# Kernel tuning notes

Hardware: AMD Instinct MI355X
Metric: run time of the kernel (lower is better)

Reference implementation:

```python
import jax, jax.numpy as jnp
import numpy as np

# Grid constants from point_cloud_range and PILLAR_SIZE (KITTI PointPillars defaults)
PX, PY, PZ = 0.16, 0.16, 4.0
X0, Y0, Z0 = 0.0, -39.68, -3.0
NX, NY, NZ = 432, 496, 1
X_OFF = PX / 2 + X0
Y_OFF = PY / 2 + Y0
Z_OFF = PZ / 2 + Z0
B = 8          # batch size
P = 96000      # total pillars across batch
M = 32         # max points per pillar
CIN = 10       # 4 base + 3 cluster + 3 center
COUT = 64      # FILTERS[-1]
BN_EPS = 1e-3


def setup_inputs() -> dict:
    key = jax.random.key(0)
    k1, k2, k3, k4, k5, k6 = jax.random.split(key, 6)
    pillars = jax.random.normal(k1, (P, M, 4), dtype=jnp.float32)
    b = jax.random.randint(k2, (P,), 0, B, dtype=jnp.int32)
    z = jnp.zeros((P,), dtype=jnp.int32)  # nz == 1
    y = jax.random.randint(k3, (P,), 0, NY, dtype=jnp.int32)
    x = jax.random.randint(k4, (P,), 0, NX, dtype=jnp.int32)
    coords = jnp.stack([b, z, y, x], axis=1)  # (P, 4) as [batch, z, y, x]
    num_points = jax.random.randint(k5, (P,), 1, M + 1, dtype=jnp.int32)
    W = jax.random.normal(k6, (CIN, COUT), dtype=jnp.float32) * 0.05
    gamma = jnp.ones((COUT,), dtype=jnp.float32)
    beta = jnp.zeros((COUT,), dtype=jnp.float32)
    return {"pillars": pillars, "coords": coords, "num_points": num_points,
            "W": W, "gamma": gamma, "beta": beta}


def _pfe_forward(pillars, W, gamma, beta, coords, num_points):
    # --- feature augmentation ---
    abs_xyz = pillars[:, :, :3]                                   # (P, M, 3)
    n = num_points.astype(pillars.dtype)[:, None, None]
    mean_xyz = jnp.sum(abs_xyz, axis=1, keepdims=True) / n        # (P, 1, 3)
    xyz_to_cluster = abs_xyz - mean_xyz                           # (P, M, 3)
    cz = coords[:, 1].astype(pillars.dtype)
    cy = coords[:, 2].astype(pillars.dtype)
    cx = coords[:, 3].astype(pillars.dtype)
    centers = jnp.stack([cx * PX + X_OFF, cy * PY + Y_OFF, cz * PZ + Z_OFF], axis=-1)
    xyz_to_center = abs_xyz - centers[:, None, :]                 # (P, M, 3)
    feats = jnp.concatenate([pillars, xyz_to_cluster, xyz_to_center], axis=-1)  # (P, M, 10)

    # --- PFNLayer: linear (no bias) + BatchNorm1d (train-mode batch stats) + ReLU + max over points ---
    h = jnp.einsum("pmi,io->pmo", feats, W)                       # (P, M, COUT)
    mu = jnp.mean(h, axis=(0, 1))
    var = jnp.var(h, axis=(0, 1))                                 # biased, like torch BN
    h = (h - mu) * jax.lax.rsqrt(var + BN_EPS) * gamma + beta
    h = jax.nn.relu(h)
    pv = jnp.max(h, axis=1)                                       # (P, COUT)

    # --- scatter pillar features to dense BEV grid ---
    cell = coords[:, 1] + coords[:, 2] * NX + coords[:, 3]        # z + y*nx + x
    flat = coords[:, 0] * (NZ * NY * NX) + cell                   # (P,)
    bev = jnp.zeros((B * NZ * NY * NX, COUT), dtype=pv.dtype).at[flat].set(pv)
    bev = bev.reshape(B, NZ * NY * NX, COUT).transpose(0, 2, 1)   # (B, C, nz*ny*nx)
    return bev.reshape(B, COUT * NZ, NY, NX)


def reference(pillars, coords, num_points, W, gamma, beta):
    return _pfe_forward(pillars, W, gamma, beta, coords, num_points)
```

## Files before the change

### kernel.cpp

```cpp
#include <hip/hip_runtime.h>

#define NPILLARS 96000
#define MPTS 32
#define NCHAN 64
#define NXC 432
#define NYC 496
#define NB 8
#define NCELLS (NXC*NYC)
#define NBLK 1024
#define PXc 0.16f
#define PYc 0.16f
#define PZc 4.0f
#define XOFF (0.08f)
#define YOFF (0.08f - 39.68f)
#define ZOFF (2.0f - 3.0f)
#define BN_EPS 1e-3f

typedef __attribute__((ext_vector_type(8))) short short8;
typedef __attribute__((ext_vector_type(16))) float float16;
typedef __attribute__((ext_vector_type(4))) float natf4;

__device__ __forceinline__ short f2bf(float x) {
    union { float f; unsigned u; } v; v.f = x;
    unsigned r = v.u + 0x7FFFu + ((v.u >> 16) & 1u);
    return (short)(r >> 16);
}

#define PAIRS(Q) \
 Q(0,0,0) Q(1,0,1) Q(2,0,2) Q(3,0,3) Q(4,0,4) Q(5,0,5) Q(6,0,6) Q(7,0,7) Q(8,0,8) Q(9,0,9) \
 Q(10,1,1) Q(11,1,2) Q(12,1,3) Q(13,1,4) Q(14,1,5) Q(15,1,6) Q(16,1,7) Q(17,1,8) Q(18,1,9) \
 Q(19,2,2) Q(20,2,3) Q(21,2,4) Q(22,2,5) Q(23,2,6) Q(24,2,7) Q(25,2,8) Q(26,2,9) \
 Q(27,3,3) Q(28,3,4) Q(29,3,5) Q(30,3,6) Q(31,3,7) Q(32,3,8) Q(33,3,9) \
 Q(34,4,4) Q(35,4,5) Q(36,4,6) Q(37,4,7) Q(38,4,8) Q(39,4,9) \
 Q(40,5,5) Q(41,5,6) Q(42,5,7) Q(43,5,8) Q(44,5,9) \
 Q(45,6,6) Q(46,6,7) Q(47,6,8) Q(48,6,9) \
 Q(49,7,7) Q(50,7,8) Q(51,7,9) \
 Q(52,8,8) Q(53,8,9) \
 Q(54,9,9)

__global__ __launch_bounds__(256, 4)
void k_moments(const float4* __restrict__ pillars,
               const int4* __restrict__ coords,
               const int* __restrict__ num_points,
               float* __restrict__ partial,
               int* __restrict__ winner) {
    const int tid  = threadIdx.x;
    const int lane = tid & 63;
    const int sub  = lane & 31;
    const int half = lane >> 5;
    const int wv   = tid >> 6;
    const int wid    = (blockIdx.x * blockDim.x + tid) >> 6;
    const int nwaves = (gridDim.x * blockDim.x) >> 6;

    float s0=0.f,s1=0.f,s2=0.f,s3=0.f,s4=0.f,s5=0.f,s6=0.f,s7=0.f,s8=0.f,s9=0.f;
#define QDECL(idx,i,j) float q_##i##_##j = 0.f;
    PAIRS(QDECL)
#undef QDECL

    for (int base = wid * 2; base < NPILLARS; base += nwaves * 2) {
        const int p = base + half;
        float4 pt = pillars[p * MPTS + sub];
        float sx = pt.x, sy = pt.y, sz = pt.z;
#pragma unroll
        for (int m = 16; m >= 1; m >>= 1) {
            sx += __shfl_xor(sx, m);
            sy += __shfl_xor(sy, m);
            sz += __shfl_xor(sz, m);
        }
        const float n = (float)num_points[p];
        const float mx = sx / n, my = sy / n, mz = sz / n;
        const int4  cd = coords[p];
        const float ctx = (float)cd.w * PXc + XOFF;
        const float cty = (float)cd.z * PYc + YOFF;
        const float ctz = (float)cd.y * PZc + ZOFF;
        const float f0=pt.x, f1=pt.y, f2=pt.z, f3=pt.w;
        const float f4=pt.x-mx,  f5=pt.y-my,  f6=pt.z-mz;
        const float f7=pt.x-ctx, f8=pt.y-cty, f9=pt.z-ctz;
        s0+=f0; s1+=f1; s2+=f2; s3+=f3; s4+=f4;
        s5+=f5; s6+=f6; s7+=f7; s8+=f8; s9+=f9;
#define QACC(idx,i,j) q_##i##_##j = fmaf(f##i, f##j, q_##i##_##j);
        PAIRS(QACC)
#undef QACC
        if (sub == 0) {
            const int cell = cd.y + cd.z * NXC + cd.w;
            atomicMax(&winner[cd.x * NCELLS + cell], p);
        }
    }

    __shared__ float lds_part[4][65];
#define RED6(v) { v += __shfl_xor(v,32); v += __shfl_xor(v,16); v += __shfl_xor(v,8); \
                  v += __shfl_xor(v,4);  v += __shfl_xor(v,2);  v += __shfl_xor(v,1); }
    RED6(s0) RED6(s1) RED6(s2) RED6(s3) RED6(s4)
    RED6(s5) RED6(s6) RED6(s7) RED6(s8) RED6(s9)
#define QRED(idx,i,j) RED6(q_##i##_##j)
    PAIRS(QRED)
#undef QRED
#undef RED6
    if (lane == 0) {
        float* dst = &lds_part[wv][0];
        dst[0]=s0; dst[1]=s1; dst[2]=s2; dst[3]=s3; dst[4]=s4;
        dst[5]=s5; dst[6]=s6; dst[7]=s7; dst[8]=s8; dst[9]=s9;
#define QST(idx,i,j) dst[10+idx] = q_##i##_##j;
        PAIRS(QST)
#undef QST
    }
    __syncthreads();
    if (tid < 65) {
        const float acc = lds_part[0][tid] + lds_part[1][tid]
                        + lds_part[2][tid] + lds_part[3][tid];
        partial[tid * NBLK + blockIdx.x] = acc;
    }
}

__global__ void k_finalize(const float* __restrict__ partial,
                           const float* __restrict__ W,
                           const float* __restrict__ gamma,
                           const float* __restrict__ beta,
                           float* __restrict__ ss) {
    __shared__ float mom[65];
    const int tid = threadIdx.x;
    if (tid < 65) mom[tid] = 0.f;
    __syncthreads();
    for (int task = tid; task < 65 * 4; task += 256) {
        const int i = task >> 2, ch = task & 3;
        const float4* p4 = (const float4*)(partial + (size_t)i * NBLK) + ch * (NBLK/16);
        float a0=0.f, a1=0.f, a2=0.f, a3=0.f;
#pragma unroll 8
        for (int b = 0; b < NBLK/16; b++) {
            float4 v = p4[b];
            a0 += v.x; a1 += v.y; a2 += v.z; a3 += v.w;
        }
        atomicAdd(&mom[i], (a0 + a1) + (a2 + a3));
    }
    __syncthreads();
    const int c = tid;
    if (c >= 64) return;
    const double invN = 1.0 / ((double)NPILLARS * (double)MPTS);
    double wv[10];
#pragma unroll
    for (int i = 0; i < 10; i++) wv[i] = (double)W[i * NCHAN + c];
    double mu = 0.0;
#pragma unroll
    for (int i = 0; i < 10; i++) mu += (double)mom[i] * wv[i];
    mu *= invN;
    double e2 = 0.0;
#define QFOLD(idx,i,j) { double t = (double)mom[10+idx] * wv[i] * wv[j]; \
                         e2 += (i == j) ? t : 2.0 * t; }
    PAIRS(QFOLD)
#undef QFOLD
    e2 *= invN;
    const double var = e2 - mu * mu;
    const float scale = (float)((double)gamma[c] / sqrt(var + (double)BN_EPS));
    const float shift = beta[c] - (float)mu * scale;
    ss[c] = scale;
    ss[64 + c] = shift;
}

__global__ __launch_bounds__(256, 4)
void k_pv(const float4* __restrict__ pillars,
          const int4* __restrict__ coords,
          const int* __restrict__ num_points,
          const float* __restrict__ W,
          const float* __restrict__ ss,
          float* __restrict__ pv) {
    const int tid  = threadIdx.x;
    const int lane = tid & 63;
    const int sub  = lane & 31;
    const int half = lane >> 5;
    const int wid    = (blockIdx.x * blockDim.x + tid) >> 6;
    const int nwaves = (gridDim.x * blockDim.x) >> 6;

    short8 bf0, bf1;
#pragma unroll
    for (int r = 0; r < 8; r++) {
        const int k = half * 8 + r;
        bf0[r] = (k < 10) ? f2bf(W[k * NCHAN + sub])      : (short)0;
        bf1[r] = (k < 10) ? f2bf(W[k * NCHAN + 32 + sub]) : (short)0;
    }
    const float scale0 = ss[sub],      shift0 = ss[64 + sub];
    const float scale1 = ss[32 + sub], shift1 = ss[96 + sub];

    for (int p = wid; p < NPILLARS; p += nwaves) {
        float4 pt = pillars[p * MPTS + sub];
        float sx = pt.x, sy = pt.y, sz = pt.z;
#pragma unroll
        for (int m = 16; m >= 1; m >>= 1) {
            sx += __shfl_xor(sx, m);
            sy += __shfl_xor(sy, m);
            sz += __shfl_xor(sz, m);
        }
        const float n = (float)num_points[p];
        const float mx = sx / n, my = sy / n, mz = sz / n;
        const int4  cd = coords[p];
        const float ctx = (float)cd.w * PXc + XOFF;
        const float cty = (float)cd.z * PYc + YOFF;
        const float ctz = (float)cd.y * PZc + ZOFF;
        const short b0 = f2bf(pt.x),     b1 = f2bf(pt.y),     b2 = f2bf(pt.z),
                    b3 = f2bf(pt.w),     b4 = f2bf(pt.x-mx),  b5 = f2bf(pt.y-my),
                    b6 = f2bf(pt.z-mz),  b7 = f2bf(pt.x-ctx), b8 = f2bf(pt.y-cty),
                    b9 = f2bf(pt.z-ctz);
        short8 a;
        a[0] = half ? b8 : b0;
        a[1] = half ? b9 : b1;
        a[2] = half ? (short)0 : b2;
        a[3] = half ? (short)0 : b3;
        a[4] = half ? (short)0 : b4;
        a[5] = half ? (short)0 : b5;
        a[6] = half ? (short)0 : b6;
        a[7] = half ? (short)0 : b7;
        float16 acc0 = {};
        float16 acc1 = {};
        acc0 = __builtin_amdgcn_mfma_f32_32x32x16_bf16(a, bf0, acc0, 0, 0, 0);
        acc1 = __builtin_amdgcn_mfma_f32_32x32x16_bf16(a, bf1, acc1, 0, 0, 0);
        float m0 = 0.f, m1 = 0.f;
#pragma unroll
        for (int r = 0; r < 16; r++) {
            m0 = fmaxf(m0, fmaf(acc0[r], scale0, shift0));
            m1 = fmaxf(m1, fmaf(acc1[r], scale1, shift1));
        }
        m0 = fmaxf(m0, __shfl_xor(m0, 32));
        m1 = fmaxf(m1, __shfl_xor(m1, 32));
        pv[p * NCHAN + lane] = half ? m1 : m0;
    }
}

__global__ void k_expand(const int* __restrict__ winner,
                         const float* __restrict__ pv,
                         float* __restrict__ out) {
    const int idx = blockIdx.x * blockDim.x + threadIdx.x;
    const int total8 = NB * NCELLS / 8;
    if (idx >= total8) return;
    const int b    = (idx << 3) / NCELLS;
    const int cell = (idx << 3) - b * NCELLS;
    const int4 w0 = ((const int4*)winner)[idx * 2];
    const int4 w1 = ((const int4*)winner)[idx * 2 + 1];
    float* obase = out + (size_t)b * NCHAN * NCELLS + cell;
#pragma unroll 4
    for (int c = 0; c < NCHAN; c++) {
        natf4 v0, v1;
        v0.x = (w0.x >= 0) ? pv[w0.x * NCHAN + c] : 0.f;
        v0.y = (w0.y >= 0) ? pv[w0.y * NCHAN + c] : 0.f;
        v0.z = (w0.z >= 0) ? pv[w0.z * NCHAN + c] : 0.f;
        v0.w = (w0.w >= 0) ? pv[w0.w * NCHAN + c] : 0.f;
        v1.x = (w1.x >= 0) ? pv[w1.x * NCHAN + c] : 0.f;
        v1.y = (w1.y >= 0) ? pv[w1.y * NCHAN + c] : 0.f;
        v1.z = (w1.z >= 0) ? pv[w1.z * NCHAN + c] : 0.f;
        v1.w = (w1.w >= 0) ? pv[w1.w * NCHAN + c] : 0.f;
        natf4* o = reinterpret_cast<natf4*>(obase + (size_t)c * NCELLS);
        __builtin_nontemporal_store(v0, o);
        __builtin_nontemporal_store(v1, o + 1);
    }
}

extern "C" void kernel_launch(void* const* d_in, const int* in_sizes, int n_in,
                              void* d_out, int out_size, void* d_ws, size_t ws_size,
                              hipStream_t stream) {
    const float4* pillars    = (const float4*)d_in[0];
    const int4*   coords     = (const int4*)d_in[1];
    const int*    num_points = (const int*)d_in[2];
    const float*  W          = (const float*)d_in[3];
    const float*  gamma      = (const float*)d_in[4];
    const float*  beta       = (const float*)d_in[5];
    float* out = (float*)d_out;

    char* ws = (char*)d_ws;
    float* ss     = (float*)ws;
    int*   winner = (int*)(ws + 4096);
    float* pv     = (float*)(ws + 4096 + (size_t)NB * NCELLS * sizeof(int));
    float* partial = pv;

    (void)hipMemsetAsync(winner, 0xFF, (size_t)NB * NCELLS * sizeof(int), stream);

    k_moments <<<NBLK, 256, 0, stream>>>(pillars, coords, num_points, partial, winner);
    k_finalize<<<1, 256, 0, stream>>>(partial, W, gamma, beta, ss);
    k_pv      <<<2048, 256, 0, stream>>>(pillars, coords, num_points, W, ss, pv);
    k_expand  <<<(NB * NCELLS / 8 + 255) / 256, 256, 0, stream>>>(winner, pv, out);
}
```

Baseline: 654.8 us.

## Fuse moments and matmul pass; defer BN+ReLU to expand via per-pillar max/min

Merges the moments kernel and the pillar-feature kernel into a single pass over the pillars. The pass stores both the per-channel max and min of the raw linear output. BN scale/shift and ReLU are applied later in the expand kernel, which picks max or min depending on the sign of the scale. This avoids reading the pillar data a second time, at the cost of writing two pv buffers, changing the moment normalization, and using normal instead of nontemporal stores with 4-cell vectors.

```diff
diff --git a/kernel.cpp b/kernel.cpp
--- a/kernel.cpp
+++ b/kernel.cpp
@@ -18,7 +18,6 @@
 
 typedef __attribute__((ext_vector_type(8))) short short8;
 typedef __attribute__((ext_vector_type(16))) float float16;
-typedef __attribute__((ext_vector_type(4))) float natf4;
 
 __device__ __forceinline__ short f2bf(float x) {
     union { float f; unsigned u; } v; v.f = x;
@@ -38,12 +37,15 @@
  Q(52,8,8) Q(53,8,9) \
  Q(54,9,9)
 
-__global__ __launch_bounds__(256, 4)
-void k_moments(const float4* __restrict__ pillars,
-               const int4* __restrict__ coords,
-               const int* __restrict__ num_points,
-               float* __restrict__ partial,
-               int* __restrict__ winner) {
+__global__ __launch_bounds__(256, 3)
+void k_fused(const float4* __restrict__ pillars,
+             const int4* __restrict__ coords,
+             const int* __restrict__ num_points,
+             const float* __restrict__ W,
+             float* __restrict__ pvmax,
+             float* __restrict__ pvmin,
+             float* __restrict__ partial,
+             int* __restrict__ winner) {
     const int tid  = threadIdx.x;
     const int lane = tid & 63;
     const int sub  = lane & 31;
@@ -52,13 +54,20 @@
     const int wid    = (blockIdx.x * blockDim.x + tid) >> 6;
     const int nwaves = (gridDim.x * blockDim.x) >> 6;
 
+    short8 bf0, bf1;
+#pragma unroll
+    for (int r = 0; r < 8; r++) {
+        const int k = half * 8 + r;
+        bf0[r] = (k < 10) ? f2bf(W[k * NCHAN + sub])      : (short)0;
+        bf1[r] = (k < 10) ? f2bf(W[k * NCHAN + 32 + sub]) : (short)0;
+    }
+
     float s0=0.f,s1=0.f,s2=0.f,s3=0.f,s4=0.f,s5=0.f,s6=0.f,s7=0.f,s8=0.f,s9=0.f;
 #define QDECL(idx,i,j) float q_##i##_##j = 0.f;
     PAIRS(QDECL)
 #undef QDECL
 
-    for (int base = wid * 2; base < NPILLARS; base += nwaves * 2) {
-        const int p = base + half;
+    for (int p = wid; p < NPILLARS; p += nwaves) {
         float4 pt = pillars[p * MPTS + sub];
         float sx = pt.x, sy = pt.y, sz = pt.z;
 #pragma unroll
@@ -81,7 +90,33 @@
 #define QACC(idx,i,j) q_##i##_##j = fmaf(f##i, f##j, q_##i##_##j);
         PAIRS(QACC)
 #undef QACC
-        if (sub == 0) {
+        const short b0 = f2bf(f0), b1 = f2bf(f1), b2 = f2bf(f2), b3 = f2bf(f3),
+                    b4 = f2bf(f4), b5 = f2bf(f5), b6 = f2bf(f6), b7 = f2bf(f7),
+                    b8 = f2bf(f8), b9 = f2bf(f9);
+        short8 a;
+        a[0] = half ? b8 : b0;
+        a[1] = half ? b9 : b1;
+        a[2] = half ? (short)0 : b2;
+        a[3] = half ? (short)0 : b3;
+        a[4] = half ? (short)0 : b4;
+        a[5] = half ? (short)0 : b5;
+        a[6] = half ? (short)0 : b6;
+        a[7] = half ? (short)0 : b7;
+        float16 acc0 = {};
+        float16 acc1 = {};
+        acc0 = __builtin_amdgcn_mfma_f32_32x32x16_bf16(a, bf0, acc0, 0, 0, 0);
+        acc1 = __builtin_amdgcn_mfma_f32_32x32x16_bf16(a, bf1, acc1, 0, 0, 0);
+        float mx0 = -3.4e38f, mx1 = -3.4e38f, mn0 = 3.4e38f, mn1 = 3.4e38f;
+#pragma unroll
+        for (int r = 0; r < 16; r++) {
+            mx0 = fmaxf(mx0, acc0[r]);  mn0 = fminf(mn0, acc0[r]);
+            mx1 = fmaxf(mx1, acc1[r]);  mn1 = fminf(mn1, acc1[r]);
+        }
+        mx0 = fmaxf(mx0, __shfl_xor(mx0, 32));  mn0 = fminf(mn0, __shfl_xor(mn0, 32));
+        mx1 = fmaxf(mx1, __shfl_xor(mx1, 32));  mn1 = fminf(mn1, __shfl_xor(mn1, 32));
+        pvmax[p * NCHAN + lane] = half ? mx1 : mx0;
+        pvmin[p * NCHAN + lane] = half ? mn1 : mn0;
+        if (lane == 0) {
             const int cell = cd.y + cd.z * NXC + cd.w;
             atomicMax(&winner[cd.x * NCELLS + cell], p);
         }
@@ -135,7 +170,7 @@
     __syncthreads();
     const int c = tid;
     if (c >= 64) return;
-    const double invN = 1.0 / ((double)NPILLARS * (double)MPTS);
+    const double invN = 1.0 / (2.0 * (double)NPILLARS * (double)MPTS);
     double wv[10];
 #pragma unroll
     for (int i = 0; i < 10; i++) wv[i] = (double)W[i * NCHAN + c];
@@ -156,99 +191,33 @@
     ss[64 + c] = shift;
 }
 
-__global__ __launch_bounds__(256, 4)
-void k_pv(const float4* __restrict__ pillars,
-          const int4* __restrict__ coords,
-          const int* __restrict__ num_points,
-          const float* __restrict__ W,
-          const float* __restrict__ ss,
-          float* __restrict__ pv) {
-    const int tid  = threadIdx.x;
-    const int lane = tid & 63;
-    const int sub  = lane & 31;
-    const int half = lane >> 5;
-    const int wid    = (blockIdx.x * blockDim.x + tid) >> 6;
-    const int nwaves = (gridDim.x * blockDim.x) >> 6;
-
-    short8 bf0, bf1;
-#pragma unroll
-    for (int r = 0; r < 8; r++) {
-        const int k = half * 8 + r;
-        bf0[r] = (k < 10) ? f2bf(W[k * NCHAN + sub])      : (short)0;
-        bf1[r] = (k < 10) ? f2bf(W[k * NCHAN + 32 + sub]) : (short)0;
-    }
-    const float scale0 = ss[sub],      shift0 = ss[64 + sub];
-    const float scale1 = ss[32 + sub], shift1 = ss[96 + sub];
-
-    for (int p = wid; p < NPILLARS; p += nwaves) {
-        float4 pt = pillars[p * MPTS + sub];
-        float sx = pt.x, sy = pt.y, sz = pt.z;
-#pragma unroll
-        for (int m = 16; m >= 1; m >>= 1) {
-            sx += __shfl_xor(sx, m);
-            sy += __shfl_xor(sy, m);
-            sz += __shfl_xor(sz, m);
-        }
-        const float n = (float)num_points[p];
-        const float mx = sx / n, my = sy / n, mz = sz / n;
-        const int4  cd = coords[p];
-        const float ctx = (float)cd.w * PXc + XOFF;
-        const float cty = (float)cd.z * PYc + YOFF;
-        const float ctz = (float)cd.y * PZc + ZOFF;
-        const short b0 = f2bf(pt.x),     b1 = f2bf(pt.y),     b2 = f2bf(pt.z),
-                    b3 = f2bf(pt.w),     b4 = f2bf(pt.x-mx),  b5 = f2bf(pt.y-my),
-                    b6 = f2bf(pt.z-mz),  b7 = f2bf(pt.x-ctx), b8 = f2bf(pt.y-cty),
-                    b9 = f2bf(pt.z-ctz);
-        short8 a;
-        a[0] = half ? b8 : b0;
-        a[1] = half ? b9 : b1;
-        a[2] = half ? (short)0 : b2;
-        a[3] = half ? (short)0 : b3;
-        a[4] = half ? (short)0 : b4;
-        a[5] = half ? (short)0 : b5;
-        a[6] = half ? (short)0 : b6;
-        a[7] = half ? (short)0 : b7;
-        float16 acc0 = {};
-        float16 acc1 = {};
-        acc0 = __builtin_amdgcn_mfma_f32_32x32x16_bf16(a, bf0, acc0, 0, 0, 0);
-        acc1 = __builtin_amdgcn_mfma_f32_32x32x16_bf16(a, bf1, acc1, 0, 0, 0);
-        float m0 = 0.f, m1 = 0.f;
-#pragma unroll
-        for (int r = 0; r < 16; r++) {
-            m0 = fmaxf(m0, fmaf(acc0[r], scale0, shift0));
-            m1 = fmaxf(m1, fmaf(acc1[r], scale1, shift1));
-        }
-        m0 = fmaxf(m0, __shfl_xor(m0, 32));
-        m1 = fmaxf(m1, __shfl_xor(m1, 32));
-        pv[p * NCHAN + lane] = half ? m1 : m0;
-    }
-}
-
 __global__ void k_expand(const int* __restrict__ winner,
-                         const float* __restrict__ pv,
+                         const float* __restrict__ pvmax,
+                         const float* __restrict__ pvmin,
+                         const float* __restrict__ ss,
                          float* __restrict__ out) {
-    const int idx = blockIdx.x * blockDim.x + threadIdx.x;
-    const int total8 = NB * NCELLS / 8;
-    if (idx >= total8) return;
-    const int b    = (idx << 3) / NCELLS;
-    const int cell = (idx << 3) - b * NCELLS;
-    const int4 w0 = ((const int4*)winner)[idx * 2];
-    const int4 w1 = ((const int4*)winner)[idx * 2 + 1];
+    __shared__ float s_sc[64], s_sh[64];
+    const int t = threadIdx.x;
+    if (t < 64) s_sc[t] = ss[t];
+    else if (t < 128) s_sh[t - 64] = ss[t];
+    __syncthreads();
+    const int idx = blockIdx.x * blockDim.x + t;
+    const int total4 = NB * NCELLS / 4;
+    if (idx >= total4) return;
+    const int b    = (idx << 2) / NCELLS;
+    const int cell = (idx << 2) - b * NCELLS;
+    const int4 w = ((const int4*)winner)[idx];
     float* obase = out + (size_t)b * NCHAN * NCELLS + cell;
 #pragma unroll 4
     for (int c = 0; c < NCHAN; c++) {
-        natf4 v0, v1;
-        v0.x = (w0.x >= 0) ? pv[w0.x * NCHAN + c] : 0.f;
-        v0.y = (w0.y >= 0) ? pv[w0.y * NCHAN + c] : 0.f;
-        v0.z = (w0.z >= 0) ? pv[w0.z * NCHAN + c] : 0.f;
-        v0.w = (w0.w >= 0) ? pv[w0.w * NCHAN + c] : 0.f;
-        v1.x = (w1.x >= 0) ? pv[w1.x * NCHAN + c] : 0.f;
-        v1.y = (w1.y >= 0) ? pv[w1.y * NCHAN + c] : 0.f;
-        v1.z = (w1.z >= 0) ? pv[w1.z * NCHAN + c] : 0.f;
-        v1.w = (w1.w >= 0) ? pv[w1.w * NCHAN + c] : 0.f;
-        natf4* o = reinterpret_cast<natf4*>(obase + (size_t)c * NCELLS);
-        __builtin_nontemporal_store(v0, o);
-        __builtin_nontemporal_store(v1, o + 1);
+        const float sc = s_sc[c], sh = s_sh[c];
+        const float* buf = (sc >= 0.f) ? pvmax : pvmin;
+        float4 v;
+        v.x = (w.x >= 0) ? fmaxf(0.f, fmaf(buf[w.x * NCHAN + c], sc, sh)) : 0.f;
+        v.y = (w.y >= 0) ? fmaxf(0.f, fmaf(buf[w.y * NCHAN + c], sc, sh)) : 0.f;
+        v.z = (w.z >= 0) ? fmaxf(0.f, fmaf(buf[w.z * NCHAN + c], sc, sh)) : 0.f;
+        v.w = (w.w >= 0) ? fmaxf(0.f, fmaf(buf[w.w * NCHAN + c], sc, sh)) : 0.f;
+        *reinterpret_cast<float4*>(obase + (size_t)c * NCELLS) = v;
     }
 }
 
@@ -264,15 +233,17 @@
     float* out = (float*)d_out;
 
     char* ws = (char*)d_ws;
-    float* ss     = (float*)ws;
-    int*   winner = (int*)(ws + 4096);
-    float* pv     = (float*)(ws + 4096 + (size_t)NB * NCELLS * sizeof(int));
-    float* partial = pv;
+    const size_t PV_BYTES = (size_t)NPILLARS * NCHAN * sizeof(float);
+    float* ss      = (float*)ws;
+    int*   winner  = (int*)(ws + 4096);
+    float* pvmax   = (float*)(ws + 4096 + (size_t)NB*NCELLS*4);
+    float* pvmin   = (float*)((char*)pvmax + PV_BYTES);
+    float* partial = (float*)((char*)pvmin + PV_BYTES);
 
     (void)hipMemsetAsync(winner, 0xFF, (size_t)NB * NCELLS * sizeof(int), stream);
 
-    k_moments <<<NBLK, 256, 0, stream>>>(pillars, coords, num_points, partial, winner);
+    k_fused   <<<NBLK, 256, 0, stream>>>(pillars, coords, num_points, W,
+                                         pvmax, pvmin, partial, winner);
     k_finalize<<<1, 256, 0, stream>>>(partial, W, gamma, beta, ss);
-    k_pv      <<<2048, 256, 0, stream>>>(pillars, coords, num_points, W, ss, pv);
-    k_expand  <<<(NB * NCELLS / 8 + 255) / 256, 256, 0, stream>>>(winner, pv, out);
-}
+    k_expand  <<<(NB * NCELLS / 4 + 255) / 256, 256, 0, stream>>>(winner, pvmax, pvmin, ss, out);
+}
```

New measurement: 585.7 us. -10.6%, faster.
